# Performance work log

Measured on AMD Instinct MI355X. Metric: run time of the kernel, lower is better.

The kernel has to match this reference:

```python
import jax, jax.numpy as jnp
import numpy as np

B, T, H, W = 2, 8, 14, 14
S = H * W
DIM, HEADS = 768, 12
HD = DIM // HEADS  # 64


def setup_inputs() -> dict:
    key = jax.random.key(0)
    ks = jax.random.split(key, 6)
    std = 0.02
    return {
        "x": jax.random.normal(ks[0], (B, T, S, DIM), jnp.float32),
        "qkv_w": jax.random.normal(ks[1], (3 * DIM, DIM), jnp.float32) * std,
        "proj_w": jax.random.normal(ks[2], (DIM, DIM), jnp.float32) * std,
        "proj_b": jnp.zeros((DIM,), jnp.float32),
        "rel_pos_h": jax.random.normal(ks[3], (2 * H - 1, HD), jnp.float32) * std,
        "rel_pos_w": jax.random.normal(ks[4], (2 * W - 1, HD), jnp.float32) * std,
        "rel_pos_t": jax.random.normal(ks[5], (2 * T - 1, HD), jnp.float32) * std,
    }


def _rel_table(rel_pos, q_len):
    # q_len == k_len here, so get_rel_pos is identity and indices simplify
    idx = np.arange(q_len)[:, None] - np.arange(q_len)[None, :] + (q_len - 1)
    return rel_pos[idx]  # [q_len, k_len, head_dim]


def reference(x, qkv_w, proj_w, proj_b, rel_pos_h, rel_pos_w, rel_pos_t):
    B_, T_, S_, C = x.shape
    H_ = W_ = int(S_ ** 0.5)
    N = T_ * S_
    hd = C // HEADS
    scale = hd ** -0.5

    xf = x.reshape(B_, N, C)
    qkv = (xf @ qkv_w.T).reshape(B_, N, 3, HEADS, hd).transpose(2, 0, 3, 1, 4)
    q, k, v = qkv[0], qkv[1], qkv[2]  # each [B, heads, N, hd]

    attn = jnp.einsum('bhqd,bhkd->bhqk', q, k) * scale  # [B, heads, N, N]

    # Decomposed relative-position bias (note: uses UNscaled q, as in original)
    r_q = q.reshape(B_, HEADS, T_, H_, W_, hd)
    Rh = _rel_table(rel_pos_h, H_)  # [H, H, hd]
    Rw = _rel_table(rel_pos_w, W_)  # [W, W, hd]
    Rt = _rel_table(rel_pos_t, T_)  # [T, T, hd]
    rel_h = jnp.einsum('bythwc,hkc->bythwk', r_q, Rh)
    rel_w = jnp.einsum('bythwc,wkc->bythwk', r_q, Rw)
    rel_t = jnp.einsum('bythwc,tkc->bythwk', r_q, Rt)

    attn = (attn.reshape(B_, HEADS, T_, H_, W_, T_, H_, W_)
            + rel_h[:, :, :, :, :, None, :, None]
            + rel_w[:, :, :, :, :, None, None, :]
            + rel_t[:, :, :, :, :, :, None, None]
            ).reshape(B_, HEADS, N, N)

    attn = jax.nn.softmax(attn, axis=-1)
    out = jnp.einsum('bhqk,bhkd->bhqd', attn, v)  # [B, heads, N, hd]
    out = out.transpose(0, 2, 1, 3).reshape(B_, N, C)
    out = out @ proj_w.T + proj_b
    return out.reshape(B_, T_, S_, C)
```

## Files before the change

### kernel.cpp

```cpp
#include <hip/hip_runtime.h>

using f16   = _Float16;
using f16x4 = __attribute__((ext_vector_type(4))) _Float16;
using f16x8 = __attribute__((ext_vector_type(8))) _Float16;
using f32x4 = __attribute__((ext_vector_type(4))) float;
using u32x4 = __attribute__((ext_vector_type(4))) unsigned int;
using fp16x2_raw = __fp16 __attribute__((ext_vector_type(2)));

#define MFMA16(a, b, c) __builtin_amdgcn_mfma_f32_16x16x32_f16((a), (b), (c), 0, 0, 0)

namespace {
constexpr int kT = 8, kWd = 14, kS = 196;
constexpr int kN = 1568;
constexpr int kM = 3136;
constexpr int kHeads = 12;
constexpr int kNp = 1664;
constexpr float kLog2e = 1.4426950408889634f;
constexpr size_t OFF_WH   = 0;
constexpr size_t OFF_WP   = 3538944;
constexpr size_t OFF_Q    = 4718592;
constexpr size_t OFF_XH   = 9830400;
constexpr size_t OFF_KF   = 14942208;
constexpr size_t OFF_KONE = 20054016;
constexpr size_t OFF_VSWZ = 20267008;
constexpr size_t WS_TOTAL = 25378816;
constexpr int kKoneTot = 13 * 8 * 2 * 64 * 8;

__device__ inline f16x4 pack4(float4 v) {
  union { fp16x2_raw h2[2]; f16x4 f4; } u;
  u.h2[0] = __builtin_amdgcn_cvt_pkrtz(v.x, v.y);
  u.h2[1] = __builtin_amdgcn_cvt_pkrtz(v.z, v.w);
  return u.f4;
}

__device__ inline float fast_exp2(float x) {
#if __has_builtin(__builtin_amdgcn_exp2f)
  return __builtin_amdgcn_exp2f(x);
#else
  return __expf(x * 0.6931471805599453f);
#endif
}

__device__ inline void gload_lds16(const f16* g, f16* l) {
  __builtin_amdgcn_global_load_lds(
      (const __attribute__((address_space(1))) unsigned int*)g,
      (__attribute__((address_space(3))) unsigned int*)l,
      16, 0, 0);
}

__device__ inline float dotqLDS(const f16x8* qh, const f16* Rrow) {
  float s = 0.f;
#pragma unroll
  for (int i = 0; i < 8; ++i) {
    f16x8 a = qh[i];
    f16x8 b = *(const f16x8*)(Rrow + i * 8);
#pragma unroll
    for (int k = 0; k < 8; ++k) s += (float)a[k] * (float)b[k];
  }
  return s;
}
}

__global__ __launch_bounds__(256) void arp_kone(f16* __restrict__ konefrag) {
  int g = blockIdx.x * 256 + threadIdx.x;
  if (g < kKoneTot) {
    int j = g & 7;
    int lane = (g >> 3) & 63;
    int s2 = (g >> 9) & 1;
    int nt = (g >> 10) & 7;
    int kt = g >> 13;
    int slot = lane & 15, qd = lane >> 4;
    int kin = (nt >> 1) * 32 + (slot >> 2) * 8 + (nt & 1) * 4 + (slot & 3);
    int key = kt * 128 + kin;
    int c = s2 * 32 + qd * 8 + j;
    int t2 = key / kS; int rm = key - t2 * kS;
    int h2 = rm / kWd; int w2 = rm - h2 * kWd;
    if (t2 > kT - 1) t2 = kT - 1;
    float v = 0.f;
    if (c == h2) v = 1.f;
    else if (c == 14 + w2) v = 1.f;
    else if (c == 28 + t2) v = 1.f;
    else if (c == 36 && key >= kN) v = 1.f;
    konefrag[g] = (f16)v;
  }
}

__global__ __launch_bounds__(256, 2) void arp_gemm_qkv(
    const float* __restrict__ X, const float* __restrict__ qkvw,
    f16* __restrict__ qf, f16* __restrict__ kfrag, f16* __restrict__ vswz) {
  __shared__ char smem[34816];
  f16* sA = (f16*)smem;
  f16* sB = (f16*)(smem + 10240);
  f16* sE = (f16*)smem;
  const int tid = threadIdx.x, lane = tid & 63, wv = tid >> 6;
  const int m0 = blockIdx.y * 128, n0 = blockIdx.x * 128;
  const int wm = (wv & 1) * 64, wn = (wv >> 1) * 64;
  const int frow = lane & 15, quad = lane >> 4, fcol = quad * 8;
  const f32x4 vzero = {0.f, 0.f, 0.f, 0.f};
  f32x4 acc[4][4];
#pragma unroll
  for (int i = 0; i < 4; ++i)
#pragma unroll
    for (int j = 0; j < 4; ++j) acc[i][j] = vzero;

  float4 pA[2][2], pB[2][2];
#pragma unroll
  for (int i = 0; i < 2; ++i) {
    int idx = i * 256 + tid;
    int r = idx >> 2, c8 = (idx & 3) * 8;
    int gm = m0 + r; if (gm >= kM) gm = kM - 1;
    pA[i][0] = *(const float4*)(X + (size_t)gm * 768 + c8);
    pA[i][1] = *(const float4*)(X + (size_t)gm * 768 + c8 + 4);
    pB[i][0] = *(const float4*)(qkvw + (size_t)(n0 + r) * 768 + c8);
    pB[i][1] = *(const float4*)(qkvw + (size_t)(n0 + r) * 768 + c8 + 4);
  }

  for (int kt = 0; kt < 24; ++kt) {
#pragma unroll
    for (int i = 0; i < 2; ++i) {
      int idx = i * 256 + tid;
      int r = idx >> 2, c8 = (idx & 3) * 8;
      union { f16x4 h[2]; u32x4 u; } ua, ub;
      ua.h[0] = pack4(pA[i][0]); ua.h[1] = pack4(pA[i][1]);
      ub.h[0] = pack4(pB[i][0]); ub.h[1] = pack4(pB[i][1]);
      *(u32x4*)&sA[r * 40 + c8] = ua.u;
      *(u32x4*)&sB[r * 40 + c8] = ub.u;
    }
    __syncthreads();
    if (kt < 23) {
      int ko = (kt + 1) * 32;
#pragma unroll
      for (int i = 0; i < 2; ++i) {
        int idx = i * 256 + tid;
        int r = idx >> 2, c8 = (idx & 3) * 8;
        int gm = m0 + r; if (gm >= kM) gm = kM - 1;
        pA[i][0] = *(const float4*)(X + (size_t)gm * 768 + ko + c8);
        pA[i][1] = *(const float4*)(X + (size_t)gm * 768 + ko + c8 + 4);
        pB[i][0] = *(const float4*)(qkvw + (size_t)(n0 + r) * 768 + ko + c8);
        pB[i][1] = *(const float4*)(qkvw + (size_t)(n0 + r) * 768 + ko + c8 + 4);
      }
    }
    f16x8 af[4], bf[4];
#pragma unroll
    for (int t = 0; t < 4; ++t) {
      af[t] = *(const f16x8*)&sA[(wm + t * 16 + frow) * 40 + fcol];
      bf[t] = *(const f16x8*)&sB[(wn + t * 16 + frow) * 40 + fcol];
    }
#pragma unroll
    for (int mt = 0; mt < 4; ++mt)
#pragma unroll
      for (int nt = 0; nt < 4; ++nt)
        acc[mt][nt] = MFMA16(af[mt], bf[nt], acc[mt][nt]);
    __syncthreads();
  }

  const int which = n0 / 768;
  if (which == 2) {
#pragma unroll
    for (int mt = 0; mt < 4; ++mt)
#pragma unroll
      for (int nt = 0; nt < 4; ++nt) {
        int cl = wn + nt * 16 + frow;
#pragma unroll
        for (int rg = 0; rg < 4; ++rg) {
          int rl = wm + mt * 16 + quad * 4 + rg;
          sE[cl * 136 + rl] = (f16)acc[mt][nt][rg];
        }
      }
    __syncthreads();
    int cl = tid >> 1;
    int rb = (tid & 1) * 64;
    int rem = n0 + cl - 1536;
    int hh = rem >> 6, d = rem & 63;
    int td = d >> 4, fr = d & 15;
#pragma unroll
    for (int j = 0; j < 8; ++j) {
      int ms = m0 + rb + j * 8;
      if (ms < kM) {
        int bb2 = (ms >= kN) ? 1 : 0;
        int ns = ms - bb2 * kN;
        int bh = bb2 * kHeads + hh;
        int kt2 = ns >> 7, kr = ns & 127;
        int kc = kr >> 5, qd = (kr >> 3) & 3;
        f16* dst = vswz + ((((size_t)(bh * 13 + kt2)) * 4 + td) * 4 + kc) * 512
                        + (qd * 16 + fr) * 8;
        *(u32x4*)dst = *(const u32x4*)&sE[cl * 136 + rb + j * 8];
      }
    }
  } else {
#pragma unroll
    for (int mt = 0; mt < 4; ++mt) {
      int rbase = m0 + wm + mt * 16 + quad * 4;
#pragma unroll
      for (int nt = 0; nt < 4; ++nt) {
        int col0 = n0 + wn + nt * 16;
        int rem = col0 - which * 768;
        int hh = rem >> 6;
        int d = (rem & 63) + frow;
        int s = d >> 5, qd2 = (d >> 3) & 3, j = d & 7;
#pragma unroll
        for (int rg = 0; rg < 4; ++rg) {
          int m = rbase + rg;
          if (m < kM) {
            int bb2 = (m >= kN) ? 1 : 0;
            int ns = m - bb2 * kN;
            int bh = bb2 * kHeads + hh;
            float av = acc[mt][nt][rg];
            if (which == 0) {
              av *= kLog2e;
              qf[((size_t)bh * kNp + ns) * 64 + d] = (f16)av;
            } else {
              av *= 0.125f;
              int kt2 = ns >> 7;
              int kin = ns & 127;
              int nt2 = ((kin >> 5) << 1) | ((kin >> 2) & 1);
              int slot = ((kin >> 3) & 3) * 4 + (kin & 3);
              kfrag[(((size_t)(bh * 13 + kt2) * 8 + nt2) * 2 + s) * 512
                    + (qd2 * 16 + slot) * 8 + j] = (f16)av;
            }
          }
        }
      }
    }
  }
}

__global__ __launch_bounds__(256, 3) void arp_attn(
    const f16* qf,
    const float* __restrict__ Rh, const float* __restrict__ Rw, const float* __restrict__ Rt,
    const f16* __restrict__ kfrag, const f16* __restrict__ konefrag,
    const f16* __restrict__ vswz, f16* qfO) {
  __shared__ char pool[49152];
  f16* sKa = (f16*)pool;
  f16* sKb = (f16*)(pool + 16384);
  f16* sV  = (f16*)(pool + 32768);
  f16* sQE = (f16*)pool;
  f16* sR  = (f16*)(pool + 8192);

  const int tid = threadIdx.x, lane = tid & 63, wv = tid >> 6;
  const int Lb  = blockIdx.y * 25 + blockIdx.x;
  const int Lw  = (Lb & 7) * 75 + (Lb >> 3);
  const int q0 = (Lw % 25) * 64;
  const int bh = Lw / 25;
  const int frow = lane & 15, quad = lane >> 4;
  const f32x4 vzero = {0.f, 0.f, 0.f, 0.f};

  const f16* kba = kfrag + (size_t)bh * 13 * 8192;
  const f16* vba = vswz + (size_t)bh * 13 * 8192;

  for (int g = tid; g < 69 * 16; g += 256) {
    int row = g >> 4, c4 = (g & 15) * 4;
    const float* src = (row < 27) ? Rh + row * 64 + c4
                     : (row < 54) ? Rw + (row - 27) * 64 + c4
                                  : Rt + (row - 54) * 64 + c4;
    *(f16x4*)&sR[row * 72 + c4] = pack4(*(const float4*)src);
  }
  __syncthreads();

  {
    int q = q0 + lane;
    int qc = (q < kN) ? q : kN - 1;
    int tq = qc / kS, sr = qc - tq * kS;
    int hq = sr / kWd, wq = sr - hq * kWd;
    if (wv < 3) {
      f16x8 qh[8];
      const f16x8* qv8 = (const f16x8*)(qf + ((size_t)bh * kNp + q) * 64);
#pragma unroll
      for (int i = 0; i < 8; ++i) qh[i] = qv8[i];
      if (wv == 0) {
#pragma unroll
        for (int e = 0; e < 14; ++e)
          sQE[lane * 64 + e] = (f16)dotqLDS(qh, &sR[(hq - e + 13) * 72]);
      } else if (wv == 1) {
#pragma unroll
        for (int e = 0; e < 14; ++e)
          sQE[lane * 64 + 14 + e] = (f16)dotqLDS(qh, &sR[(wq - e + 40) * 72]);
      } else {
#pragma unroll
        for (int e = 0; e < 8; ++e)
          sQE[lane * 64 + 28 + e] = (f16)dotqLDS(qh, &sR[(tq - e + 61) * 72]);
      }
    } else {
      sQE[lane * 64 + 36] = (f16)(-30000.f);
#pragma unroll
      for (int e = 37; e < 64; ++e) sQE[lane * 64 + e] = (f16)0.f;
    }
  }
  __syncthreads();

  f16x8 aQ0, aQ1, aQE0, aQE1;
  {
    int row = q0 + wv * 16 + frow;
    const f16* qp = qf + ((size_t)bh * kNp + row) * 64;
    aQ0 = *(const f16x8*)(qp + quad * 8);
    aQ1 = *(const f16x8*)(qp + 32 + quad * 8);
    int rl = wv * 16 + frow;
    aQE0 = *(const f16x8*)&sQE[rl * 64 + quad * 8];
    aQE1 = *(const f16x8*)&sQE[rl * 64 + 32 + quad * 8];
  }
  __syncthreads();

#pragma unroll
  for (int i = 0; i < 4; ++i) {
    int u = (i * 256 + tid) * 8;
    gload_lds16(kba + u, sKa + u);
    gload_lds16(konefrag + u, sKb + u);
    gload_lds16(vba + u, sV + u);
  }

  float den = 0.f;
  f32x4 Oc[4];
#pragma unroll
  for (int t = 0; t < 4; ++t) Oc[t] = vzero;

  for (int kt = 0; kt < 13; ++kt) {
    __syncthreads();

    f32x4 Sc[8];
    __builtin_amdgcn_s_setprio(1);
#pragma unroll
    for (int nt = 0; nt < 8; ++nt) {
      const f16* ka = &sKa[nt * 1024 + lane * 8];
      const f16* kb = &sKb[nt * 1024 + lane * 8];
      f32x4 s = MFMA16(*(const f16x8*)(ka), aQ0, vzero);
      s = MFMA16(*(const f16x8*)(ka + 512), aQ1, s);
      s = MFMA16(*(const f16x8*)(kb), aQE0, s);
      Sc[nt] = MFMA16(*(const f16x8*)(kb + 512), aQE1, s);
    }
    __builtin_amdgcn_s_setprio(0);
    f16x8 bV[4][4];
#pragma unroll
    for (int td = 0; td < 4; ++td)
#pragma unroll
      for (int kc = 0; kc < 4; ++kc)
        bV[td][kc] = *(const f16x8*)&sV[(td * 4 + kc) * 512 + lane * 8];
    __syncthreads();

    if (kt < 12) {
      const f16* kfa = kba + (size_t)(kt + 1) * 8192;
      const f16* koa = konefrag + (size_t)(kt + 1) * 8192;
      const f16* vfa = vba + (size_t)(kt + 1) * 8192;
#pragma unroll
      for (int i = 0; i < 4; ++i) {
        int u = (i * 256 + tid) * 8;
        gload_lds16(kfa + u, sKa + u);
        gload_lds16(koa + u, sKb + u);
        gload_lds16(vfa + u, sV + u);
      }
    }

#pragma unroll
    for (int nt = 0; nt < 8; ++nt)
#pragma unroll
      for (int r = 0; r < 4; ++r)
        Sc[nt][r] = fast_exp2(Sc[nt][r]);

    __builtin_amdgcn_s_setprio(1);
#pragma unroll
    for (int kc = 0; kc < 4; ++kc) {
      union { _Float16 h[8]; f16x8 v; } up;
#pragma unroll
      for (int r = 0; r < 4; ++r) {
        up.h[r]     = (f16)Sc[2 * kc][r];
        up.h[4 + r] = (f16)Sc[2 * kc + 1][r];
      }
#pragma unroll
      for (int r = 0; r < 4; ++r)
        den += (float)up.h[r] + (float)up.h[4 + r];
#pragma unroll
      for (int td = 0; td < 4; ++td)
        Oc[td] = MFMA16(up.v, bV[td][kc], Oc[td]);
    }
    __builtin_amdgcn_s_setprio(0);
  }

  den += __shfl_xor(den, 16, 64);
  den += __shfl_xor(den, 32, 64);
  float lr[4];
#pragma unroll
  for (int r = 0; r < 4; ++r)
    lr[r] = 1.f / __shfl(den, quad * 4 + r, 64);
#pragma unroll
  for (int td = 0; td < 4; ++td)
#pragma unroll
    for (int r = 0; r < 4; ++r) {
      int row = q0 + wv * 16 + quad * 4 + r;
      if (row < kN) {
        float val = Oc[td][r] * lr[r];
        qfO[((size_t)bh * kNp + row) * 64 + td * 16 + frow] = (f16)val;
      }
    }
}

__global__ __launch_bounds__(256, 4) void arp_gemm_proj(
    const f16* A, const float* __restrict__ projw,
    const float* __restrict__ bias, float* __restrict__ out) {
  __shared__ f16 sA[64 * 40];
  __shared__ f16 sB[128 * 40];
  const int tid = threadIdx.x, lane = tid & 63, wv = tid >> 6;
  const int m0 = blockIdx.y * 64, n0 = blockIdx.x * 128;
  const int frow = lane & 15, quad = lane >> 4, fcol = quad * 8;
  const f32x4 vzero = {0.f, 0.f, 0.f, 0.f};
  f32x4 acc[8];
#pragma unroll
  for (int j = 0; j < 8; ++j) acc[j] = vzero;

  u32x4 pA;
  float4 pB[2][2];
  {
    int r = tid >> 2, c8 = (tid & 3) * 8;
    int m = m0 + r;
    int bb = (m >= kN) ? 1 : 0;
    int ns = m - bb * kN;
    pA = *(const u32x4*)(A + ((size_t)(bb * kHeads) * kNp + ns) * 64 + c8);
#pragma unroll
    for (int i = 0; i < 2; ++i) {
      int idx = i * 256 + tid;
      int rb2 = idx >> 2, cb8 = (idx & 3) * 8;
      pB[i][0] = *(const float4*)(projw + (size_t)(n0 + rb2) * 768 + cb8);
      pB[i][1] = *(const float4*)(projw + (size_t)(n0 + rb2) * 768 + cb8 + 4);
    }
  }

  for (int kt = 0; kt < 24; ++kt) {
    {
      int r = tid >> 2, c8 = (tid & 3) * 8;
      *(u32x4*)&sA[r * 40 + c8] = pA;
#pragma unroll
      for (int i = 0; i < 2; ++i) {
        int idx = i * 256 + tid;
        int rb2 = idx >> 2, cb8 = (idx & 3) * 8;
        union { f16x4 h[2]; u32x4 u; } ub;
        ub.h[0] = pack4(pB[i][0]); ub.h[1] = pack4(pB[i][1]);
        *(u32x4*)&sB[rb2 * 40 + cb8] = ub.u;
      }
    }
    __syncthreads();
    if (kt < 23) {
      int k1 = kt + 1;
      int hd = k1 >> 1, dof = (k1 & 1) * 32;
      int r = tid >> 2, c8 = (tid & 3) * 8;
      int m = m0 + r;
      int bb = (m >= kN) ? 1 : 0;
      int ns = m - bb * kN;
      pA = *(const u32x4*)(A + ((size_t)(bb * kHeads + hd) * kNp + ns) * 64 + dof + c8);
#pragma unroll
      for (int i = 0; i < 2; ++i) {
        int idx = i * 256 + tid;
        int rb2 = idx >> 2, cb8 = (idx & 3) * 8;
        pB[i][0] = *(const float4*)(projw + (size_t)(n0 + rb2) * 768 + k1 * 32 + cb8);
        pB[i][1] = *(const float4*)(projw + (size_t)(n0 + rb2) * 768 + k1 * 32 + cb8 + 4);
      }
    }
    f16x8 af = *(const f16x8*)&sA[(wv * 16 + frow) * 40 + fcol];
    f16x8 bf[8];
#pragma unroll
    for (int u = 0; u < 8; ++u)
      bf[u] = *(const f16x8*)&sB[(u * 16 + frow) * 40 + fcol];
#pragma unroll
    for (int u = 0; u < 8; ++u)
      acc[u] = MFMA16(af, bf[u], acc[u]);
    __syncthreads();
  }
#pragma unroll
  for (int u = 0; u < 8; ++u) {
    int col = n0 + u * 16 + frow;
    float bv = bias[col];
#pragma unroll
    for (int rg = 0; rg < 4; ++rg) {
      int m = m0 + wv * 16 + quad * 4 + rg;
      out[(size_t)m * 768 + col] = acc[u][rg] + bv;
    }
  }
}

extern "C" void kernel_launch(void* const* d_in, const int* in_sizes, int n_in,
                              void* d_out, int out_size, void* d_ws, size_t ws_size,
                              hipStream_t stream) {
  if (ws_size < WS_TOTAL) return;
  const float* x      = (const float*)d_in[0];
  const float* qkv_w  = (const float*)d_in[1];
  const float* proj_w = (const float*)d_in[2];
  const float* proj_b = (const float*)d_in[3];
  const float* rph    = (const float*)d_in[4];
  const float* rpw    = (const float*)d_in[5];
  const float* rpt    = (const float*)d_in[6];
  char* ws = (char*)d_ws;
  f16* qf       = (f16*)(ws + OFF_Q);
  f16* kfrag    = (f16*)(ws + OFF_KF);
  f16* konefrag = (f16*)(ws + OFF_KONE);
  f16* vswz     = (f16*)(ws + OFF_VSWZ);

  arp_kone<<<(kKoneTot + 255) / 256, 256, 0, stream>>>(konefrag);
  arp_gemm_qkv<<<dim3(18, 25), 256, 0, stream>>>(x, qkv_w, qf, kfrag, vswz);
  arp_attn<<<dim3(25, 24), 256, 0, stream>>>(qf, rph, rpw, rpt, kfrag, konefrag, vswz, qf);
  arp_gemm_proj<<<dim3(6, 49), 256, 0, stream>>>(qf, proj_w, proj_b, (float*)d_out);
}
```

Before: 168.8 us.

## Fuse kone setup into QKV GEMM, add XCD block remap, shrink proj tile

Removes the separate kone-fragment kernel by computing it at the start of the QKV GEMM blocks, saving a launch. Both GEMMs remap block IDs so that consecutive tiles land on the same XCD, which is meant to improve L2 locality. The projection GEMM tile is narrowed from 128 to 64 columns, doubling the grid to improve CU occupancy at the cost of reloading A tiles twice as often.

```diff
diff --git a/kernel.cpp b/kernel.cpp
--- a/kernel.cpp
+++ b/kernel.cpp
@@ -16,10 +16,7 @@
 constexpr int kHeads = 12;
 constexpr int kNp = 1664;
 constexpr float kLog2e = 1.4426950408889634f;
-constexpr size_t OFF_WH   = 0;
-constexpr size_t OFF_WP   = 3538944;
 constexpr size_t OFF_Q    = 4718592;
-constexpr size_t OFF_XH   = 9830400;
 constexpr size_t OFF_KF   = 14942208;
 constexpr size_t OFF_KONE = 20054016;
 constexpr size_t OFF_VSWZ = 20267008;
@@ -61,39 +58,46 @@
 }
 }
 
-__global__ __launch_bounds__(256) void arp_kone(f16* __restrict__ konefrag) {
-  int g = blockIdx.x * 256 + threadIdx.x;
-  if (g < kKoneTot) {
-    int j = g & 7;
-    int lane = (g >> 3) & 63;
-    int s2 = (g >> 9) & 1;
-    int nt = (g >> 10) & 7;
-    int kt = g >> 13;
-    int slot = lane & 15, qd = lane >> 4;
-    int kin = (nt >> 1) * 32 + (slot >> 2) * 8 + (nt & 1) * 4 + (slot & 3);
-    int key = kt * 128 + kin;
-    int c = s2 * 32 + qd * 8 + j;
-    int t2 = key / kS; int rm = key - t2 * kS;
-    int h2 = rm / kWd; int w2 = rm - h2 * kWd;
-    if (t2 > kT - 1) t2 = kT - 1;
-    float v = 0.f;
-    if (c == h2) v = 1.f;
-    else if (c == 14 + w2) v = 1.f;
-    else if (c == 28 + t2) v = 1.f;
-    else if (c == 36 && key >= kN) v = 1.f;
-    konefrag[g] = (f16)v;
-  }
-}
-
 __global__ __launch_bounds__(256, 2) void arp_gemm_qkv(
     const float* __restrict__ X, const float* __restrict__ qkvw,
-    f16* __restrict__ qf, f16* __restrict__ kfrag, f16* __restrict__ vswz) {
+    f16* __restrict__ qf, f16* __restrict__ kfrag, f16* __restrict__ vswz,
+    f16* __restrict__ konefrag) {
   __shared__ char smem[34816];
   f16* sA = (f16*)smem;
   f16* sB = (f16*)(smem + 10240);
   f16* sE = (f16*)smem;
   const int tid = threadIdx.x, lane = tid & 63, wv = tid >> 6;
-  const int m0 = blockIdx.y * 128, n0 = blockIdx.x * 128;
+
+  {
+    int g = (blockIdx.y * 18 + blockIdx.x) * 256 + tid;
+    if (g < kKoneTot) {
+      int j = g & 7;
+      int ln = (g >> 3) & 63;
+      int s2 = (g >> 9) & 1;
+      int nt = (g >> 10) & 7;
+      int kt = g >> 13;
+      int slot = ln & 15, qd = ln >> 4;
+      int kin = (nt >> 1) * 32 + (slot >> 2) * 8 + (nt & 1) * 4 + (slot & 3);
+      int key = kt * 128 + kin;
+      int c = s2 * 32 + qd * 8 + j;
+      int t2 = key / kS; int rm = key - t2 * kS;
+      int h2 = rm / kWd; int w2 = rm - h2 * kWd;
+      if (t2 > kT - 1) t2 = kT - 1;
+      float v = 0.f;
+      if (c == h2) v = 1.f;
+      else if (c == 14 + w2) v = 1.f;
+      else if (c == 28 + t2) v = 1.f;
+      else if (c == 36 && key >= kN) v = 1.f;
+      konefrag[g] = (f16)v;
+    }
+  }
+
+  int orig = blockIdx.y * 18 + blockIdx.x;
+  int xcd = orig & 7;
+  int base = (xcd < 2) ? xcd * 57 : 2 * 57 + (xcd - 2) * 56;
+  int wgid = base + (orig >> 3);
+  const int m0 = (wgid / 18) * 128, n0 = (wgid % 18) * 128;
+
   const int wm = (wv & 1) * 64, wn = (wv >> 1) * 64;
   const int frow = lane & 15, quad = lane >> 4, fcol = quad * 8;
   const f32x4 vzero = {0.f, 0.f, 0.f, 0.f};
@@ -396,44 +400,40 @@
     const f16* A, const float* __restrict__ projw,
     const float* __restrict__ bias, float* __restrict__ out) {
   __shared__ f16 sA[64 * 40];
-  __shared__ f16 sB[128 * 40];
+  __shared__ f16 sB[64 * 40];
   const int tid = threadIdx.x, lane = tid & 63, wv = tid >> 6;
-  const int m0 = blockIdx.y * 64, n0 = blockIdx.x * 128;
+
+  int orig = blockIdx.y * 12 + blockIdx.x;
+  int xcd = orig & 7;
+  int base = (xcd < 4) ? xcd * 74 : 4 * 74 + (xcd - 4) * 73;
+  int wgid = base + (orig >> 3);
+  const int m0 = (wgid / 12) * 64, n0 = (wgid % 12) * 64;
+
   const int frow = lane & 15, quad = lane >> 4, fcol = quad * 8;
   const f32x4 vzero = {0.f, 0.f, 0.f, 0.f};
-  f32x4 acc[8];
-#pragma unroll
-  for (int j = 0; j < 8; ++j) acc[j] = vzero;
+  f32x4 acc[4];
+#pragma unroll
+  for (int j = 0; j < 4; ++j) acc[j] = vzero;
 
   u32x4 pA;
-  float4 pB[2][2];
+  float4 pB[2];
   {
     int r = tid >> 2, c8 = (tid & 3) * 8;
     int m = m0 + r;
     int bb = (m >= kN) ? 1 : 0;
     int ns = m - bb * kN;
     pA = *(const u32x4*)(A + ((size_t)(bb * kHeads) * kNp + ns) * 64 + c8);
-#pragma unroll
-    for (int i = 0; i < 2; ++i) {
-      int idx = i * 256 + tid;
-      int rb2 = idx >> 2, cb8 = (idx & 3) * 8;
-      pB[i][0] = *(const float4*)(projw + (size_t)(n0 + rb2) * 768 + cb8);
-      pB[i][1] = *(const float4*)(projw + (size_t)(n0 + rb2) * 768 + cb8 + 4);
-    }
+    pB[0] = *(const float4*)(projw + (size_t)(n0 + r) * 768 + c8);
+    pB[1] = *(const float4*)(projw + (size_t)(n0 + r) * 768 + c8 + 4);
   }
 
   for (int kt = 0; kt < 24; ++kt) {
     {
       int r = tid >> 2, c8 = (tid & 3) * 8;
       *(u32x4*)&sA[r * 40 + c8] = pA;
-#pragma unroll
-      for (int i = 0; i < 2; ++i) {
-        int idx = i * 256 + tid;
-        int rb2 = idx >> 2, cb8 = (idx & 3) * 8;
-        union { f16x4 h[2]; u32x4 u; } ub;
-        ub.h[0] = pack4(pB[i][0]); ub.h[1] = pack4(pB[i][1]);
-        *(u32x4*)&sB[rb2 * 40 + cb8] = ub.u;
-      }
+      union { f16x4 h[2]; u32x4 u; } ub;
+      ub.h[0] = pack4(pB[0]); ub.h[1] = pack4(pB[1]);
+      *(u32x4*)&sB[r * 40 + c8] = ub.u;
     }
     __syncthreads();
     if (kt < 23) {
@@ -444,26 +444,21 @@
       int bb = (m >= kN) ? 1 : 0;
       int ns = m - bb * kN;
       pA = *(const u32x4*)(A + ((size_t)(bb * kHeads + hd) * kNp + ns) * 64 + dof + c8);
-#pragma unroll
-      for (int i = 0; i < 2; ++i) {
-        int idx = i * 256 + tid;
-        int rb2 = idx >> 2, cb8 = (idx & 3) * 8;
-        pB[i][0] = *(const float4*)(projw + (size_t)(n0 + rb2) * 768 + k1 * 32 + cb8);
-        pB[i][1] = *(const float4*)(projw + (size_t)(n0 + rb2) * 768 + k1 * 32 + cb8 + 4);
-      }
+      pB[0] = *(const float4*)(projw + (size_t)(n0 + r) * 768 + k1 * 32 + c8);
+      pB[1] = *(const float4*)(projw + (size_t)(n0 + r) * 768 + k1 * 32 + c8 + 4);
     }
     f16x8 af = *(const f16x8*)&sA[(wv * 16 + frow) * 40 + fcol];
-    f16x8 bf[8];
-#pragma unroll
-    for (int u = 0; u < 8; ++u)
+    f16x8 bf[4];
+#pragma unroll
+    for (int u = 0; u < 4; ++u)
       bf[u] = *(const f16x8*)&sB[(u * 16 + frow) * 40 + fcol];
 #pragma unroll
-    for (int u = 0; u < 8; ++u)
+    for (int u = 0; u < 4; ++u)
       acc[u] = MFMA16(af, bf[u], acc[u]);
     __syncthreads();
   }
 #pragma unroll
-  for (int u = 0; u < 8; ++u) {
+  for (int u = 0; u < 4; ++u) {
     int col = n0 + u * 16 + frow;
     float bv = bias[col];
 #pragma unroll
@@ -491,8 +486,7 @@
   f16* konefrag = (f16*)(ws + OFF_KONE);
   f16* vswz     = (f16*)(ws + OFF_VSWZ);
 
-  arp_kone<<<(kKoneTot + 255) / 256, 256, 0, stream>>>(konefrag);
-  arp_gemm_qkv<<<dim3(18, 25), 256, 0, stream>>>(x, qkv_w, qf, kfrag, vswz);
+  arp_gemm_qkv<<<dim3(18, 25), 256, 0, stream>>>(x, qkv_w, qf, kfrag, vswz, konefrag);
   arp_attn<<<dim3(25, 24), 256, 0, stream>>>(qf, rph, rpw, rpt, kfrag, konefrag, vswz, qf);
-  arp_gemm_proj<<<dim3(6, 49), 256, 0, stream>>>(qf, proj_w, proj_b, (float*)d_out);
-}
+  arp_gemm_proj<<<dim3(12, 49), 256, 0, stream>>>(qf, proj_w, proj_b, (float*)d_out);
+}
```

After: 161.3 us, median of 2. -4.4%, faster.
